# Performance work log

Measured on AMD Instinct MI355X. Metric: run time of the kernel, lower is better.

Reference implementation:

```python
import jax, jax.numpy as jnp
import numpy as np

B, T = 4, 512
IN, OUT, D, HID = 80, 4096, 512, 1024
E, NB, LPB = 4, 2, 4
NL = NB * LPB
H, M = 8, 64
LB, LA, SL, SR = 4, 1, 2, 1


def setup_inputs():
    key = jax.random.key(0)
    it = iter(jax.random.split(key, 40))
    def nrm(shape, s=0.02):
        return jax.random.normal(next(it), shape, jnp.float32) * s
    return {
        'x': jax.random.normal(next(it), (B, T, IN), jnp.float32),
        'seq_len': jax.random.randint(next(it), (B,), T // 2, T + 1),
        'emb_w1': nrm((IN, HID)), 'emb_b1': jnp.zeros((HID,), jnp.float32),
        'emb_w2': nrm((HID, D)), 'emb_wo': nrm((D, OUT)),
        'f0_w1': nrm((E, IN, HID)), 'f0_b1': jnp.zeros((E, HID), jnp.float32),
        'f0_w2': nrm((E, HID, D)), 'f0_router': nrm((D, E)),
        'f0_fb': nrm((LB, D), 0.1), 'f0_fa': nrm((LA, D), 0.1),
        'f_w1': nrm((NL - 1, E, D, HID)), 'f_b1': jnp.zeros((NL - 1, E, HID), jnp.float32),
        'f_w2': nrm((NL - 1, E, HID, D)), 'f_router': nrm((NL - 1, D, E)),
        'f_fb': nrm((NL - 1, LB, D), 0.1), 'f_fa': nrm((NL - 1, LA, D), 0.1),
        'attn_wq': nrm((NB, D, D)), 'attn_wk': nrm((NB, D, D)),
        'attn_wv': nrm((NB, D, D)), 'attn_wo': nrm((NB, D, D)),
        'attn_mk': nrm((NB, M, D)), 'attn_mv': nrm((NB, M, D)),
        'ln_g': jnp.ones((NB, D), jnp.float32), 'ln_b': jnp.zeros((NB, D), jnp.float32),
        'out_w': nrm((D, OUT)), 'out_b': jnp.zeros((OUT,), jnp.float32),
    }


def _fsmn_memory(p, fb, fa):
    # m[t] = p[t] + sum_k fb[k]*p[t-(k+1)*SL] + sum_j fa[j]*p[t+(j+1)*SR]  (depthwise)
    m = p
    for k in range(fb.shape[0]):
        off = (k + 1) * SL
        past = jnp.pad(p, ((0, 0), (off, 0), (0, 0)))[:, :p.shape[1]]
        m = m + past * fb[k]
    for j in range(fa.shape[0]):
        off = (j + 1) * SR
        fut = jnp.pad(p, ((0, 0), (0, off), (0, 0)))[:, off:]
        m = m + fut * fa[j]
    return m


def _pe(dtype):
    pos = jnp.arange(T, dtype=jnp.float32)[:, None]
    div = jnp.exp(jnp.arange(0, D, 2, dtype=jnp.float32) * (-np.log(10000.0) / D))
    pe = jnp.zeros((T, D), jnp.float32)
    pe = pe.at[:, 0::2].set(jnp.sin(pos * div)).at[:, 1::2].set(jnp.cos(pos * div))
    return pe.astype(dtype)


def _layernorm(x, g, b):
    mu = jnp.mean(x, -1, keepdims=True)
    var = jnp.var(x, -1, keepdims=True)
    return (x - mu) * jax.lax.rsqrt(var + 1e-5) * g + b


def reference(x, seq_len, emb_w1, emb_b1, emb_w2, emb_wo,
              f0_w1, f0_b1, f0_w2, f0_router, f0_fb, f0_fa,
              f_w1, f_b1, f_w2, f_router, f_fb, f_fa,
              attn_wq, attn_wk, attn_wv, attn_wo, attn_mk, attn_mv,
              ln_g, ln_b, out_w, out_b):
    tok_mask = jnp.arange(T)[None, :] < seq_len[:, None]  # [B,T] valid frames

    # embed sub-network (router features; detached as in Net.forward)
    embed = jax.nn.relu(x @ emb_w1 + emb_b1) @ emb_w2      # [B,T,D]
    embed_out = embed @ emb_wo                             # [B,T,OUT]
    embed_r = jax.lax.stop_gradient(embed)

    def moe_fsmn(xi, w1, b1, w2, router, fb, fa, skip):
        gates = jax.nn.softmax(embed_r @ router, axis=-1)  # [B,T,E]
        g = jnp.max(gates, axis=-1)
        disp = jax.nn.one_hot(jnp.argmax(gates, -1), E, dtype=xi.dtype) * g[..., None]
        h = jax.nn.relu(jnp.einsum('bti,eih->beth', xi, w1) + b1[None, :, None, :])
        p = jnp.einsum('beth,ehd->betd', h, w2)            # low-rank expert proj
        p = jnp.einsum('bte,betd->btd', disp, p)           # top-1 combine
        m = _fsmn_memory(p, fb, fa)
        if skip:
            m = m + xi
        imp = jnp.sum(gates * tok_mask[..., None].astype(gates.dtype), axis=(0, 1))
        aux = jnp.var(imp) / (jnp.mean(imp) ** 2 + 1e-9)   # importance cv^2
        return m, aux

    def attention(xi, wq, wk, wv, wo, mk, mv, g, b):
        dh = D // H
        q = (xi @ wq).reshape(B, T, H, dh)
        k = jnp.concatenate([xi @ wk, jnp.broadcast_to(mk, (B, M, D))], 1).reshape(B, T + M, H, dh)
        v = jnp.concatenate([xi @ wv, jnp.broadcast_to(mv, (B, M, D))], 1).reshape(B, T + M, H, dh)
        scores = jnp.einsum('bthd,bshd->bhts', q, k) / np.sqrt(dh).astype(np.float32)
        key_ok = jnp.concatenate([tok_mask, jnp.ones((B, M), bool)], 1)  # memory keys never masked
        scores = jnp.where(key_ok[:, None, None, :], scores, jnp.float32(-1e9))
        a = jax.nn.softmax(scores, -1)
        o = jnp.einsum('bhts,bshd->bthd', a, v).reshape(B, T, D) @ wo
        return _layernorm(xi + o, g, b)

    auxes = []
    cur = x
    li = 0
    for blk in range(NB):
        for _ in range(LPB):
            if li == 0:
                cur, aux = moe_fsmn(cur, f0_w1, f0_b1, f0_w2, f0_router, f0_fb, f0_fa, False)
            else:
                j = li - 1
                cur, aux = moe_fsmn(cur, f_w1[j], f_b1[j], f_w2[j], f_router[j], f_fb[j], f_fa[j], True)
            auxes.append(aux)
            li += 1
        if blk == 0:
            cur = cur + _pe(cur.dtype)[None]
        cur = attention(cur, attn_wq[blk], attn_wk[blk], attn_wv[blk], attn_wo[blk],
                        attn_mk[blk], attn_mv[blk], ln_g[blk], ln_b[blk])
    out = cur @ out_w + out_b
    return out, embed_out, jnp.stack(auxes).sum()
```

## Files before the change

kernel.cpp:

```cpp
#include <hip/hip_runtime.h>
#include <hip/hip_bf16.h>


typedef __bf16 bf16x8 __attribute__((ext_vector_type(8)));
typedef float f32x4 __attribute__((ext_vector_type(4)));

#define B_ 4
#define T_ 512
#define IN_ 80
#define OUT_ 4096
#define D_ 512
#define HID_ 1024
#define E_ 4
#define H_ 8
#define DH_ 64
#define M_ 64
#define BT_ (B_ * T_)
#define TKV_ (T_ + M_)
#define RBLK_ (BT_ / 4)

__device__ __forceinline__ unsigned pk2(float a, float b) {
    unsigned short ua = __builtin_bit_cast(unsigned short, (__bf16)a);
    unsigned short ub = __builtin_bit_cast(unsigned short, (__bf16)b);
    return (unsigned)ua | ((unsigned)ub << 16);
}
__device__ __forceinline__ unsigned pkh2(__bf16 a, __bf16 b) {
    unsigned short ua = __builtin_bit_cast(unsigned short, a);
    unsigned short ub = __builtin_bit_cast(unsigned short, b);
    return (unsigned)ua | ((unsigned)ub << 16);
}

__global__ __launch_bounds__(256) void gemm80_k(
    const float* __restrict__ A,
    const float* __restrict__ Bw,
    const float* __restrict__ bias,
    float* __restrict__ C)
{
    __shared__ float As[80][68];
    __shared__ float Bs[80][68];
    int m0 = blockIdx.y * 64, n0 = blockIdx.x * 64;
    int tid = threadIdx.x;
#pragma unroll
    for (int i = 0; i < 5; i++) {
        int idx = tid + 256 * i;
        int m = idx / 20, c = idx % 20;
        float4 f = *(const float4*)&A[(size_t)(m0 + m) * 80 + c * 4];
        As[c * 4 + 0][m] = f.x; As[c * 4 + 1][m] = f.y;
        As[c * 4 + 2][m] = f.z; As[c * 4 + 3][m] = f.w;
    }
#pragma unroll
    for (int i = 0; i < 5; i++) {
        int idx = tid + 256 * i;
        int k = idx / 16, c = idx % 16;
        float4 f = *(const float4*)&Bw[(size_t)k * 1024 + n0 + c * 4];
        *(float4*)&Bs[k][c * 4] = f;
    }
    __syncthreads();
    int tx = tid & 15, ty = tid >> 4;
    float acc[4][4];
#pragma unroll
    for (int j = 0; j < 4; j++)
#pragma unroll
        for (int i = 0; i < 4; i++) acc[j][i] = 0.f;
#pragma unroll 8
    for (int k = 0; k < 80; k++) {
        float4 a = *(const float4*)&As[k][ty * 4];
        float4 b = *(const float4*)&Bs[k][tx * 4];
        float av[4] = {a.x, a.y, a.z, a.w};
        float bv[4] = {b.x, b.y, b.z, b.w};
#pragma unroll
        for (int j = 0; j < 4; j++)
#pragma unroll
            for (int i = 0; i < 4; i++) acc[j][i] += av[j] * bv[i];
    }
#pragma unroll
    for (int j = 0; j < 4; j++) {
        size_t row = (size_t)(m0 + ty * 4 + j);
        float4 o;
        o.x = fmaxf(acc[j][0] + bias[n0 + tx * 4 + 0], 0.f);
        o.y = fmaxf(acc[j][1] + bias[n0 + tx * 4 + 1], 0.f);
        o.z = fmaxf(acc[j][2] + bias[n0 + tx * 4 + 2], 0.f);
        o.w = fmaxf(acc[j][3] + bias[n0 + tx * 4 + 3], 0.f);
        *(float4*)&C[row * 1024 + n0 + tx * 4] = o;
    }
}

__global__ void wr2_k(const float* __restrict__ w2,
                      const float* __restrict__ r0,
                      const float* __restrict__ rl,
                      float* __restrict__ R2)
{
    int wv = threadIdx.x >> 6, lane = threadIdx.x & 63;
    int h = blockIdx.x * 4 + wv;
    const float* wrow = w2 + (size_t)h * 512;
    float w[8];
#pragma unroll
    for (int i = 0; i < 8; i++) w[i] = wrow[lane + 64 * i];
    for (int l = 0; l < 8; l++) {
        const float* rp = (l == 0) ? r0 : rl + (size_t)(l - 1) * 2048;
        double a0 = 0, a1 = 0, a2 = 0, a3 = 0;
#pragma unroll
        for (int i = 0; i < 8; i++) {
            int d = lane + 64 * i;
            float4 r = *(const float4*)&rp[d * 4];
            a0 += (double)w[i] * (double)r.x;
            a1 += (double)w[i] * (double)r.y;
            a2 += (double)w[i] * (double)r.z;
            a3 += (double)w[i] * (double)r.w;
        }
        for (int off = 32; off; off >>= 1) {
            a0 += __shfl_xor(a0, off); a1 += __shfl_xor(a1, off);
            a2 += __shfl_xor(a2, off); a3 += __shfl_xor(a3, off);
        }
        if (lane == 0) {
            float4 o = make_float4((float)a0, (float)a1, (float)a2, (float)a3);
            *(float4*)&R2[((size_t)l * 1024 + h) * 4] = o;
        }
    }
}

__global__ __launch_bounds__(256) void routerall_k(
    const float* __restrict__ h,
    const float* __restrict__ R2,
    const int* __restrict__ seq_len,
    int* __restrict__ eid,
    float* __restrict__ gatev,
    float* __restrict__ impPart)
{
    __shared__ float impLoc[4][32];
    int wv = threadIdx.x >> 6, lane = threadIdx.x & 63;
    int tok = blockIdx.x * 4 + wv;
    const float* hr = h + (size_t)tok * 1024;
    float acc[8][4];
#pragma unroll
    for (int l = 0; l < 8; l++)
#pragma unroll
        for (int e = 0; e < 4; e++) acc[l][e] = 0.f;
    for (int i = 0; i < 16; i++) {
        int d = lane + 64 * i;
        float hv = hr[d];
#pragma unroll
        for (int l = 0; l < 8; l++) {
            float4 r = *(const float4*)&R2[((size_t)l * 1024 + d) * 4];
            acc[l][0] += hv * r.x; acc[l][1] += hv * r.y;
            acc[l][2] += hv * r.z; acc[l][3] += hv * r.w;
        }
    }
    for (int off = 32; off; off >>= 1) {
#pragma unroll
        for (int l = 0; l < 8; l++)
#pragma unroll
            for (int e = 0; e < 4; e++) acc[l][e] += __shfl_xor(acc[l][e], off);
    }
    if (lane == 0) {
        int b = tok >> 9, t = tok & 511;
        bool valid = t < seq_len[b];
        for (int l = 0; l < 8; l++) {
            float lg[4] = {acc[l][0], acc[l][1], acc[l][2], acc[l][3]};
            float mx = fmaxf(fmaxf(lg[0], lg[1]), fmaxf(lg[2], lg[3]));
            float g[4], s = 0.f;
            for (int e = 0; e < 4; e++) { g[e] = expf(lg[e] - mx); s += g[e]; }
            float inv = 1.f / s;
            int am = 0; float bv = g[0];
            for (int e = 1; e < 4; e++) if (g[e] > bv) { bv = g[e]; am = e; }
            eid[l * BT_ + tok] = am;
            gatev[l * BT_ + tok] = bv * inv;
            for (int e = 0; e < 4; e++)
                impLoc[wv][l * 4 + e] = valid ? g[e] * inv : 0.f;
        }
    }
    __syncthreads();
    int tid = threadIdx.x;
    if (tid < 32) {
        float s = impLoc[0][tid] + impLoc[1][tid] + impLoc[2][tid] + impLoc[3][tid];
        impPart[(size_t)blockIdx.x * 32 + tid] = s;
    }
}

__global__ void cvtw_k(const float* __restrict__ src, __bf16* __restrict__ dst,
                       int nsh, int kpsh, int Ksrc)
{
    int idx = blockIdx.x * 256 + threadIdx.x;
    int cprsh = nsh - 3;
    int row = idx >> cprsh;
    int chunk = idx & ((1 << cprsh) - 1);
    int e = row >> kpsh, k = row & ((1 << kpsh) - 1);
    int n = chunk * 8;
    uint4 pk;
    if (k < Ksrc) {
        const float* sp = src + (((size_t)e * Ksrc + k) << nsh) + n;
        float4 f0 = *(const float4*)sp;
        float4 f1 = *(const float4*)(sp + 4);
        pk = make_uint4(pk2(f0.x, f0.y), pk2(f0.z, f0.w),
                        pk2(f1.x, f1.y), pk2(f1.z, f1.w));
    } else pk = make_uint4(0, 0, 0, 0);
    *(uint4*)&dst[(((size_t)row) << nsh) + n] = pk;
}

__global__ void gathera_k(const float* __restrict__ src, int lda,
                          const int* __restrict__ sorted,
                          __bf16* __restrict__ dst, int kpsh, int Ksrc)
{
    int idx = blockIdx.x * 256 + threadIdx.x;
    int cprsh = kpsh - 3;
    int row = idx >> cprsh;
    int chunk = idx & ((1 << cprsh) - 1);
    int k0 = chunk * 8;
    uint4 pk;
    if (k0 < Ksrc) {
        const float* sp = src + (size_t)sorted[row] * lda + k0;
        float4 f0 = *(const float4*)sp;
        float4 f1 = *(const float4*)(sp + 4);
        pk = make_uint4(pk2(f0.x, f0.y), pk2(f0.z, f0.w),
                        pk2(f1.x, f1.y), pk2(f1.z, f1.w));
    } else pk = make_uint4(0, 0, 0, 0);
    *(uint4*)&dst[((size_t)row << kpsh) + k0] = pk;
}

template<bool W1OUT>
__global__ __launch_bounds__(256) void egemm_k(
    const __bf16* __restrict__ Ag, const __bf16* __restrict__ Bh,
    const float* __restrict__ bias,
    __bf16* __restrict__ Cb, float* __restrict__ Cf,
    int N, int Kpad,
    const int* __restrict__ seg, const int* __restrict__ sorted,
    const float* __restrict__ scale)
{
    __shared__ __align__(16) __bf16 As[2][128 * 64];
    __shared__ __align__(16) __bf16 Bs[2][64 * 64];

    int e = blockIdx.z;
    int row0 = seg[e], cnt = seg[e + 1] - row0;
    int m0 = blockIdx.y * 128;
    if (m0 >= cnt) return;
    int n0 = blockIdx.x * 64;
    const __bf16* Bp = Bh + (size_t)e * Kpad * N;

    int tid = threadIdx.x;
    int arow = tid >> 1, ahalf = tid & 1;
    const __bf16* aptr = Ag + (size_t)(row0 + m0 + arow) * Kpad + ahalf * 32;
    int asb = arow * 64;
    int ac0 = ahalf * 4;
    int arx = arow & 7;
    int bn = tid & 63, bkc = tid >> 6;
    const __bf16* bptr = Bp + n0 + bn;
    int bsb = bn * 64;
    int brx = bn & 7;

    int lane = tid & 63, wid = tid >> 6;
    int wm = wid & 1, wn = wid >> 1;
    int l15 = lane & 15, quad = lane >> 4;

    int aoff[4][2], boff[2][2];
#pragma unroll
    for (int mt = 0; mt < 4; mt++) {
        int m = wm * 64 + mt * 16 + l15;
#pragma unroll
        for (int s = 0; s < 2; s++)
            aoff[mt][s] = m * 64 + (((s * 4 + quad) ^ (m & 7)) * 8);
    }
#pragma unroll
    for (int nt = 0; nt < 2; nt++) {
        int n = wn * 32 + nt * 16 + l15;
#pragma unroll
        for (int s = 0; s < 2; s++)
            boff[nt][s] = n * 64 + (((s * 4 + quad) ^ (n & 7)) * 8);
    }

    f32x4 acc[4][2];
#pragma unroll
    for (int mt = 0; mt < 4; mt++)
#pragma unroll
        for (int nt = 0; nt < 2; nt++)
#pragma unroll
            for (int r = 0; r < 4; r++) acc[mt][nt][r] = 0.f;

    uint4 rA[4]; unsigned rB[8];
    auto stage = [&](int k0) {
#pragma unroll
        for (int j = 0; j < 4; j++) rA[j] = *(const uint4*)(aptr + k0 + j * 8);
#pragma unroll
        for (int c = 0; c < 2; c++) {
            int kk = k0 + (bkc * 2 + c) * 8;
#pragma unroll
            for (int i = 0; i < 4; i++)
                rB[c * 4 + i] = pkh2(bptr[(size_t)(kk + 2 * i) * N],
                                     bptr[(size_t)(kk + 2 * i + 1) * N]);
        }
    };
    auto commit = [&](int buf) {
#pragma unroll
        for (int j = 0; j < 4; j++)
            *(uint4*)&As[buf][asb + (((ac0 + j) ^ arx) * 8)] = rA[j];
#pragma unroll
        for (int c = 0; c < 2; c++)
            *(uint4*)&Bs[buf][bsb + (((bkc * 2 + c) ^ brx) * 8)] =
                make_uint4(rB[c * 4 + 0], rB[c * 4 + 1], rB[c * 4 + 2], rB[c * 4 + 3]);
    };

    stage(0); commit(0); __syncthreads();
    int nt_ = Kpad >> 6;
    for (int t = 0; t < nt_; t++) {
        int buf = t & 1;
        if (t + 1 < nt_) stage((t + 1) << 6);
        bf16x8 af[4][2], bfr[2][2];
#pragma unroll
        for (int mt = 0; mt < 4; mt++)
#pragma unroll
            for (int s = 0; s < 2; s++)
                af[mt][s] = *(const bf16x8*)&As[buf][aoff[mt][s]];
#pragma unroll
        for (int ntx = 0; ntx < 2; ntx++)
#pragma unroll
            for (int s = 0; s < 2; s++)
                bfr[ntx][s] = *(const bf16x8*)&Bs[buf][boff[ntx][s]];
#pragma unroll
        for (int mt = 0; mt < 4; mt++)
#pragma unroll
            for (int ntx = 0; ntx < 2; ntx++)
#pragma unroll
                for (int s = 0; s < 2; s++)
                    acc[mt][ntx] = __builtin_amdgcn_mfma_f32_16x16x32_bf16(
                        af[mt][s], bfr[ntx][s], acc[mt][ntx], 0, 0, 0);
        if (t + 1 < nt_) commit(buf ^ 1);
        __syncthreads();
    }

#pragma unroll
    for (int mt = 0; mt < 4; mt++) {
#pragma unroll
        for (int r = 0; r < 4; r++) {
            int m = m0 + wm * 64 + mt * 16 + quad * 4 + r;
            if (m >= cnt) continue;
            if (W1OUT) {
                size_t ci = (size_t)(row0 + m);
#pragma unroll
                for (int ntx = 0; ntx < 2; ntx++) {
                    int col = n0 + wn * 32 + ntx * 16 + l15;
                    float v = acc[mt][ntx][r] + bias[e * N + col];
                    Cb[ci * N + col] = (__bf16)fmaxf(v, 0.f);
                }
            } else {
                int tok = sorted[row0 + m];
                float sc = scale[tok];
#pragma unroll
                for (int ntx = 0; ntx < 2; ntx++) {
                    int col = n0 + wn * 32 + ntx * 16 + l15;
                    Cf[(size_t)tok * N + col] = acc[mt][ntx][r] * sc;
                }
            }
        }
    }
}

template<bool BIAS>
__global__ __launch_bounds__(256) void dgemm_k(
    const float* __restrict__ A,
    const __bf16* __restrict__ Bh,
    const float* __restrict__ bias,
    float* __restrict__ C,
    int N, int K)
{
    __shared__ __align__(16) __bf16 As[2][128 * 64];
    __shared__ __align__(16) __bf16 Bs[2][64 * 64];

    int m0 = blockIdx.y * 128, n0 = blockIdx.x * 64;
    int tid = threadIdx.x;
    int arow = tid >> 1, ahalf = tid & 1;
    const float* aptr = A + (size_t)(m0 + arow) * K + ahalf * 32;
    int asb = arow * 64, ac0 = ahalf * 4, arx = arow & 7;
    int bn = tid & 63, bkc = tid >> 6;
    const __bf16* bptr = Bh + n0 + bn;
    int bsb = bn * 64, brx = bn & 7;

    int lane = tid & 63, wid = tid >> 6;
    int wm = wid & 1, wn = wid >> 1;
    int l15 = lane & 15, quad = lane >> 4;

    int aoff[4][2], boff[2][2];
#pragma unroll
    for (int mt = 0; mt < 4; mt++) {
        int m = wm * 64 + mt * 16 + l15;
#pragma unroll
        for (int s = 0; s < 2; s++)
            aoff[mt][s] = m * 64 + (((s * 4 + quad) ^ (m & 7)) * 8);
    }
#pragma unroll
    for (int nt = 0; nt < 2; nt++) {
        int n = wn * 32 + nt * 16 + l15;
#pragma unroll
        for (int s = 0; s < 2; s++)
            boff[nt][s] = n * 64 + (((s * 4 + quad) ^ (n & 7)) * 8);
    }

    f32x4 acc[4][2];
#pragma unroll
    for (int mt = 0; mt < 4; mt++)
#pragma unroll
        for (int nt = 0; nt < 2; nt++)
#pragma unroll
            for (int r = 0; r < 4; r++) acc[mt][nt][r] = 0.f;

    uint4 rA[4]; unsigned rB[8];
    auto stage = [&](int k0) {
#pragma unroll
        for (int j = 0; j < 4; j++) {
            float4 f0 = *(const float4*)(aptr + k0 + j * 8);
            float4 f1 = *(const float4*)(aptr + k0 + j * 8 + 4);
            rA[j] = make_uint4(pk2(f0.x, f0.y), pk2(f0.z, f0.w),
                               pk2(f1.x, f1.y), pk2(f1.z, f1.w));
        }
#pragma unroll
        for (int c = 0; c < 2; c++) {
            int kk = k0 + (bkc * 2 + c) * 8;
#pragma unroll
            for (int i = 0; i < 4; i++)
                rB[c * 4 + i] = pkh2(bptr[(size_t)(kk + 2 * i) * N],
                                     bptr[(size_t)(kk + 2 * i + 1) * N]);
        }
    };
    auto commit = [&](int buf) {
#pragma unroll
        for (int j = 0; j < 4; j++)
            *(uint4*)&As[buf][asb + (((ac0 + j) ^ arx) * 8)] = rA[j];
#pragma unroll
        for (int c = 0; c < 2; c++)
            *(uint4*)&Bs[buf][bsb + (((bkc * 2 + c) ^ brx) * 8)] =
                make_uint4(rB[c * 4 + 0], rB[c * 4 + 1], rB[c * 4 + 2], rB[c * 4 + 3]);
    };

    stage(0); commit(0); __syncthreads();
    int nt_ = K >> 6;
    for (int t = 0; t < nt_; t++) {
        int buf = t & 1;
        if (t + 1 < nt_) stage((t + 1) << 6);
        bf16x8 af[4][2], bfr[2][2];
#pragma unroll
        for (int mt = 0; mt < 4; mt++)
#pragma unroll
            for (int s = 0; s < 2; s++)
                af[mt][s] = *(const bf16x8*)&As[buf][aoff[mt][s]];
#pragma unroll
        for (int ntx = 0; ntx < 2; ntx++)
#pragma unroll
            for (int s = 0; s < 2; s++)
                bfr[ntx][s] = *(const bf16x8*)&Bs[buf][boff[ntx][s]];
#pragma unroll
        for (int mt = 0; mt < 4; mt++)
#pragma unroll
            for (int ntx = 0; ntx < 2; ntx++)
#pragma unroll
                for (int s = 0; s < 2; s++)
                    acc[mt][ntx] = __builtin_amdgcn_mfma_f32_16x16x32_bf16(
                        af[mt][s], bfr[ntx][s], acc[mt][ntx], 0, 0, 0);
        if (t + 1 < nt_) commit(buf ^ 1);
        __syncthreads();
    }

#pragma unroll
    for (int mt = 0; mt < 4; mt++) {
#pragma unroll
        for (int r = 0; r < 4; r++) {
            int m = m0 + wm * 64 + mt * 16 + quad * 4 + r;
#pragma unroll
            for (int ntx = 0; ntx < 2; ntx++) {
                int col = n0 + wn * 32 + ntx * 16 + l15;
                float v = acc[mt][ntx][r];
                if (BIAS) v += bias[col];
                C[(size_t)m * N + col] = v;
            }
        }
    }
}

#define MBM 128
#define MBN 64
#define MBK 32
#define LDAS 40

__global__ __launch_bounds__(256) void qkv_k(
    const float* __restrict__ A,
    const __bf16* __restrict__ wq, const __bf16* __restrict__ wk,
    const __bf16* __restrict__ wv,
    float* __restrict__ qo, float* __restrict__ ko, float* __restrict__ vo)
{
    __shared__ __align__(16) __bf16 As[MBM * LDAS];
    __shared__ __align__(16) __bf16 Bs[MBN * LDAS];

    int n0g = blockIdx.x * MBN;
    int which = n0g >> 9;
    int n0 = n0g & 511;
    const __bf16* Bp = (which == 0) ? wq : (which == 1) ? wk : wv;
    float* Cp = (which == 0) ? qo : (which == 1) ? ko : vo;
    int m0 = blockIdx.y * MBM;

    int tid = threadIdx.x;
    int arow = tid >> 1, ahalf = tid & 1;
    const float* aptr = A + (size_t)(m0 + arow) * D_ + ahalf * 16;
    int asw = (arow >> 3) & 3;
    int bn = tid & 63, bkc = tid >> 6;
    int bcs = bkc ^ ((bn >> 3) & 3);

    int lane = tid & 63, wid = tid >> 6;
    int wm = wid & 1, wn = wid >> 1;
    int l15 = lane & 15, quad = lane >> 4;

    int aoff[4], boff[2];
#pragma unroll
    for (int mt = 0; mt < 4; mt++) {
        int m = wm * 64 + mt * 16 + l15;
        aoff[mt] = m * LDAS + (quad ^ ((m >> 3) & 3)) * 8;
    }
#pragma unroll
    for (int nt = 0; nt < 2; nt++) {
        int n = wn * 32 + nt * 16 + l15;
        boff[nt] = n * LDAS + (quad ^ ((n >> 3) & 3)) * 8;
    }

    f32x4 acc[4][2];
#pragma unroll
    for (int mt = 0; mt < 4; mt++)
#pragma unroll
        for (int nt = 0; nt < 2; nt++)
#pragma unroll
            for (int r = 0; r < 4; r++) acc[mt][nt][r] = 0.f;

    for (int k0 = 0; k0 < D_; k0 += MBK) {
#pragma unroll
        for (int cc = 0; cc < 2; cc++) {
            float4 f0 = *(const float4*)(aptr + k0 + cc * 8);
            float4 f1 = *(const float4*)(aptr + k0 + cc * 8 + 4);
            uint4 pk = make_uint4(pk2(f0.x, f0.y), pk2(f0.z, f0.w),
                                  pk2(f1.x, f1.y), pk2(f1.z, f1.w));
            int cs = (ahalf * 2 + cc) ^ asw;
            *(uint4*)&As[arow * LDAS + cs * 8] = pk;
        }
        {
            __bf16 f[8];
            int kk = k0 + bkc * 8;
#pragma unroll
            for (int i = 0; i < 8; i++)
                f[i] = Bp[(size_t)(kk + i) * D_ + n0 + bn];
            uint4 pk = make_uint4(pkh2(f[0], f[1]), pkh2(f[2], f[3]),
                                  pkh2(f[4], f[5]), pkh2(f[6], f[7]));
            *(uint4*)&Bs[bn * LDAS + bcs * 8] = pk;
        }
        __syncthreads();
        bf16x8 af[4], bfm[2];
#pragma unroll
        for (int mt = 0; mt < 4; mt++) af[mt] = *(const bf16x8*)&As[aoff[mt]];
#pragma unroll
        for (int nt = 0; nt < 2; nt++) bfm[nt] = *(const bf16x8*)&Bs[boff[nt]];
#pragma unroll
        for (int mt = 0; mt < 4; mt++)
#pragma unroll
            for (int nt = 0; nt < 2; nt++)
                acc[mt][nt] = __builtin_amdgcn_mfma_f32_16x16x32_bf16(
                    af[mt], bfm[nt], acc[mt][nt], 0, 0, 0);
        __syncthreads();
    }

#pragma unroll
    for (int mt = 0; mt < 4; mt++) {
#pragma unroll
        for (int r = 0; r < 4; r++) {
            int mi = wm * 64 + mt * 16 + quad * 4 + r;
            int m = m0 + mi;
            size_t crow = which ? (size_t)(m + (m >> 9) * M_) : (size_t)m;
#pragma unroll
            for (int nt = 0; nt < 2; nt++) {
                int col = n0 + wn * 32 + nt * 16 + l15;
                Cp[crow * (size_t)D_ + col] = acc[mt][nt][r];
            }
        }
    }
}

__global__ void bucketall_k(const int* __restrict__ eidA, int* __restrict__ sortedA,
                            int* __restrict__ segA)
{
    __shared__ int cnt[E_]; __shared__ int cur[E_];
    int l = blockIdx.x;
    const int* eid = eidA + l * BT_;
    int* sorted = sortedA + l * BT_;
    int* seg = segA + l * 8;
    int tid = threadIdx.x;
    if (tid < E_) cnt[tid] = 0;
    __syncthreads();
    for (int t = tid; t < BT_; t += 256) atomicAdd(&cnt[eid[t]], 1);
    __syncthreads();
    if (tid == 0) {
        int o = 0;
        for (int e = 0; e < E_; e++) { seg[e] = o; cur[e] = o; o += cnt[e]; }
        seg[E_] = o;
    }
    __syncthreads();
    for (int t = tid; t < BT_; t += 256) {
        int pos = atomicAdd(&cur[eid[t]], 1);
        sorted[pos] = t;
    }
}

__global__ void fsmn_k(const float* __restrict__ p, const float* __restrict__ fb,
                       const float* __restrict__ fa, float* __restrict__ cur, int skip)
{
    int idx = blockIdx.x * 256 + threadIdx.x;
    int d = idx & 511;
    int t = (idx >> 9) & 511;
    float m = p[idx];
#pragma unroll
    for (int k = 0; k < 4; k++) {
        int tt = t - 2 * (k + 1);
        if (tt >= 0) m += fb[k * D_ + d] * p[idx - D_ * 2 * (k + 1)];
    }
    if (t + 1 < T_) m += fa[d] * p[idx + D_];
    if (skip) m += cur[idx];
    cur[idx] = m;
}

__global__ void addpe_k(float* __restrict__ cur) {
    int idx = blockIdx.x * 256 + threadIdx.x;
    int d = idx & 511, t = (idx >> 9) & 511;
    float div = expf((float)(d & ~1) * (-9.210340371976184f / (float)D_));
    float ang = (float)t * div;
    cur[idx] += (d & 1) ? cosf(ang) : sinf(ang);
}

__global__ void fillmem_k(const float* __restrict__ mk, const float* __restrict__ mv,
                          float* __restrict__ kbuf, float* __restrict__ vbuf)
{
    int idx = blockIdx.x * 256 + threadIdx.x;
    int d = idx & 511, m = (idx >> 9) & 63, b = idx >> 15;
    size_t row = (size_t)b * TKV_ + T_ + m;
    kbuf[row * D_ + d] = mk[m * D_ + d];
    vbuf[row * D_ + d] = mv[m * D_ + d];
}

#define QR 16
__global__ __launch_bounds__(256) void attn_k(
    const float* __restrict__ q, const float* __restrict__ kbuf,
    const float* __restrict__ vbuf, const int* __restrict__ seq_len,
    float* __restrict__ attno)
{
    __shared__ float kv[64 * 68];
    __shared__ float qs[QR][68];
    __shared__ float sc[QR][584];
    int b = blockIdx.z, h = blockIdx.y, t0 = blockIdx.x * QR;
    int tid = threadIdx.x, w = tid >> 6, lane = tid & 63;
    int r0 = w * 4;
#pragma unroll
    for (int i = 0; i < 4; i++) {
        int idx = tid + 256 * i;
        int r = idx >> 6, d = idx & 63;
        qs[r][d] = q[((size_t)(b * T_) + t0 + r) * D_ + h * DH_ + d] * 0.125f;
    }
    int sl = seq_len[b];
    int ntv = (sl + 63) >> 6;
    int kg = lane & 15, quad = lane >> 4;
    int myrow = r0 + quad;

    for (int ti = 0; ti <= ntv; ti++) {
        int t = (ti < ntv) ? ti : 8;
        int s0 = t * 64;
        __syncthreads();
        {
            const float* kp = kbuf + ((size_t)b * TKV_ + s0 + w * 16) * D_ + h * DH_ + lane;
#pragma unroll
            for (int jj = 0; jj < 4; jj++) {
                float4 kf;
                kf.x = kp[(jj * 4 + 0) * D_];
                kf.y = kp[(jj * 4 + 1) * D_];
                kf.z = kp[(jj * 4 + 2) * D_];
                kf.w = kp[(jj * 4 + 3) * D_];
                *(float4*)&kv[lane * 68 + w * 16 + jj * 4] = kf;
            }
        }
        __syncthreads();
        float a0 = 0, a1 = 0, a2 = 0, a3 = 0;
#pragma unroll 8
        for (int d = 0; d < 64; d++) {
            float4 kf = *(const float4*)&kv[d * 68 + kg * 4];
            float qv = qs[myrow][d];
            a0 = fmaf(qv, kf.x, a0);
            a1 = fmaf(qv, kf.y, a1);
            a2 = fmaf(qv, kf.z, a2);
            a3 = fmaf(qv, kf.w, a3);
        }
        int sb = s0 + kg * 4;
        float4 o;
        o.x = (sb + 0 >= T_ || sb + 0 < sl) ? a0 : -1e9f;
        o.y = (sb + 1 >= T_ || sb + 1 < sl) ? a1 : -1e9f;
        o.z = (sb + 2 >= T_ || sb + 2 < sl) ? a2 : -1e9f;
        o.w = (sb + 3 >= T_ || sb + 3 < sl) ? a3 : -1e9f;
        *(float4*)&sc[myrow][s0 + kg * 4] = o;
    }
    __syncthreads();

    float inv[4];
#pragma unroll
    for (int r = 0; r < 4; r++) {
        float mx = -1e30f;
        for (int ti = 0; ti <= ntv; ti++) {
            int s0 = ((ti < ntv) ? ti : 8) * 64;
            mx = fmaxf(mx, sc[r0 + r][s0 + lane]);
        }
        for (int off = 32; off; off >>= 1) mx = fmaxf(mx, __shfl_xor(mx, off));
        float sum = 0.f;
        for (int ti = 0; ti <= ntv; ti++) {
            int s0 = ((ti < ntv) ? ti : 8) * 64;
            float e2 = expf(sc[r0 + r][s0 + lane] - mx);
            sc[r0 + r][s0 + lane] = e2; sum += e2;
        }
        for (int off = 32; off; off >>= 1) sum += __shfl_xor(sum, off);
        inv[r] = 1.f / sum;
    }

    float o0 = 0, o1 = 0, o2 = 0, o3 = 0;
    for (int ti = 0; ti <= ntv; ti++) {
        int t = (ti < ntv) ? ti : 8;
        int s0 = t * 64;
        __syncthreads();
#pragma unroll
        for (int i = 0; i < 16; i++) {
            int idx = tid + 256 * i;
            int key = idx >> 6, d = idx & 63;
            kv[key * 68 + d] = vbuf[((size_t)b * TKV_ + s0 + key) * D_ + h * DH_ + d];
        }
        __syncthreads();
#pragma unroll 4
        for (int g = 0; g < 16; g++) {
            float4 p0 = *(const float4*)&sc[r0 + 0][s0 + g * 4];
            float4 p1 = *(const float4*)&sc[r0 + 1][s0 + g * 4];
            float4 p2 = *(const float4*)&sc[r0 + 2][s0 + g * 4];
            float4 p3 = *(const float4*)&sc[r0 + 3][s0 + g * 4];
            float v0 = kv[(g * 4 + 0) * 68 + lane];
            float v1 = kv[(g * 4 + 1) * 68 + lane];
            float v2 = kv[(g * 4 + 2) * 68 + lane];
            float v3 = kv[(g * 4 + 3) * 68 + lane];
            o0 += p0.x * v0 + p0.y * v1 + p0.z * v2 + p0.w * v3;
            o1 += p1.x * v0 + p1.y * v1 + p1.z * v2 + p1.w * v3;
            o2 += p2.x * v0 + p2.y * v1 + p2.z * v2 + p2.w * v3;
            o3 += p3.x * v0 + p3.y * v1 + p3.z * v2 + p3.w * v3;
        }
    }
    size_t base = ((size_t)(b * T_) + t0 + r0) * D_ + h * DH_ + lane;
    attno[base + 0 * D_] = o0 * inv[0];
    attno[base + 1 * D_] = o1 * inv[1];
    attno[base + 2 * D_] = o2 * inv[2];
    attno[base + 3 * D_] = o3 * inv[3];
}

__global__ void ln_k(const float* __restrict__ o, const float* __restrict__ g,
                     const float* __restrict__ bb, float* __restrict__ cur)
{
    int w = threadIdx.x >> 6, lane = threadIdx.x & 63;
    size_t row = (size_t)(blockIdx.x * 4 + w);
    float v[8]; float s = 0.f;
#pragma unroll
    for (int i = 0; i < 8; i++) {
        int d = lane + 64 * i;
        v[i] = cur[row * D_ + d] + o[row * D_ + d];
        s += v[i];
    }
    for (int off = 32; off; off >>= 1) s += __shfl_xor(s, off);
    float mu = s * (1.f / D_);
    float vs = 0.f;
#pragma unroll
    for (int i = 0; i < 8; i++) { float dd = v[i] - mu; vs += dd * dd; }
    for (int off = 32; off; off >>= 1) vs += __shfl_xor(vs, off);
    float rstd = rsqrtf(vs * (1.f / D_) + 1e-5f);
#pragma unroll
    for (int i = 0; i < 8; i++) {
        int d = lane + 64 * i;
        cur[row * D_ + d] = (v[i] - mu) * rstd * g[d] + bb[d];
    }
}

__global__ __launch_bounds__(256) void aux_k(const float* __restrict__ impPart,
                                             float* __restrict__ outp)
{
    __shared__ float red[8][32];
    __shared__ float imp[32];
    int tid = threadIdx.x;
    int c = tid & 31, p = tid >> 5;
    float s = 0.f;
    for (int b = p; b < RBLK_; b += 8) s += impPart[(size_t)b * 32 + c];
    red[p][c] = s;
    __syncthreads();
    if (tid < 32) {
        float t = 0.f;
#pragma unroll
        for (int i = 0; i < 8; i++) t += red[i][tid];
        imp[tid] = t;
    }
    __syncthreads();
    if (tid == 0) {
        float total = 0.f;
        for (int l = 0; l < 8; l++) {
            const float* ip = imp + l * 4;
            float m = (ip[0] + ip[1] + ip[2] + ip[3]) * 0.25f;
            float var = 0.f;
            for (int e = 0; e < 4; e++) { float d = ip[e] - m; var += d * d; }
            var *= 0.25f;
            total += var / (m * m + 1e-9f);
        }
        *outp = total;
    }
}

extern "C" void kernel_launch(void* const* d_in, const int* in_sizes, int n_in,
                              void* d_out, int out_size, void* d_ws, size_t ws_size,
                              hipStream_t stream)
{
    (void)in_sizes; (void)n_in; (void)out_size; (void)ws_size;
    const float* x        = (const float*)d_in[0];
    const int*   seqlen   = (const int*)d_in[1];
    const float* emb_w1   = (const float*)d_in[2];
    const float* emb_b1   = (const float*)d_in[3];
    const float* emb_w2   = (const float*)d_in[4];
    const float* emb_wo   = (const float*)d_in[5];
    const float* f0_w1    = (const float*)d_in[6];
    const float* f0_b1    = (const float*)d_in[7];
    const float* f0_w2    = (const float*)d_in[8];
    const float* f0_router= (const float*)d_in[9];
    const float* f0_fb    = (const float*)d_in[10];
    const float* f0_fa    = (const float*)d_in[11];
    const float* f_w1     = (const float*)d_in[12];
    const float* f_b1     = (const float*)d_in[13];
    const float* f_w2     = (const float*)d_in[14];
    const float* f_router = (const float*)d_in[15];
    const float* f_fb     = (const float*)d_in[16];
    const float* f_fa     = (const float*)d_in[17];
    const float* attn_wq  = (const float*)d_in[18];
    const float* attn_wk  = (const float*)d_in[19];
    const float* attn_wv  = (const float*)d_in[20];
    const float* attn_wo  = (const float*)d_in[21];
    const float* attn_mk  = (const float*)d_in[22];
    const float* attn_mv  = (const float*)d_in[23];
    const float* ln_g     = (const float*)d_in[24];
    const float* ln_b     = (const float*)d_in[25];
    const float* out_w    = (const float*)d_in[26];
    const float* out_b    = (const float*)d_in[27];

    float* out0 = (float*)d_out;
    float* out1 = out0 + (size_t)BT_ * OUT_;
    float* out2 = out1 + (size_t)BT_ * OUT_;

    float* fws = (float*)d_ws;
    size_t o = 0;
    float* embedF = fws + o; o += (size_t)BT_ * D_;
    float* curB   = fws + o; o += (size_t)BT_ * D_;
    float* hbuf   = fws + o; o += (size_t)BT_ * HID_;
    float* pbuf   = fws + o; o += (size_t)BT_ * D_;
    float* kbuf   = fws + o; o += (size_t)B_ * TKV_ * D_;
    float* vbuf   = fws + o; o += (size_t)B_ * TKV_ * D_;
    float* gatev  = fws + o; o += (size_t)8 * BT_;
    float* impPart= fws + o; o += (size_t)RBLK_ * 32;
    float* R2     = fws + o; o += (size_t)8 * 1024 * 4;
    int* eid     = (int*)(fws + o); o += (size_t)8 * BT_;
    int* sortedA = (int*)(fws + o); o += (size_t)8 * BT_;
    int* segA    = (int*)(fws + o); o += 64;
    __bf16* Ag    = (__bf16*)hbuf;
    __bf16* hbufh = (__bf16*)(hbuf + (size_t)BT_ * D_ / 2);
    __bf16* w1h   = (__bf16*)kbuf;
    __bf16* w2h   = (__bf16*)vbuf;
    __bf16* w2e_h = (__bf16*)vbuf;
    __bf16* woe_h = (__bf16*)kbuf;
    __bf16* outw_h= (__bf16*)kbuf;
    __bf16* wqh   = (__bf16*)embedF;
    __bf16* wkh   = wqh + (size_t)D_ * D_;
    __bf16* wvh   = wkh + (size_t)D_ * D_;
    __bf16* woh   = wvh + (size_t)D_ * D_;
    float* qbuf  = pbuf;
    float* attno = hbuf;
    float* tmpo  = hbuf + (size_t)BT_ * D_;

    gemm80_k<<<dim3(HID_ / 64, BT_ / 64, 1), 256, 0, stream>>>(x, emb_w1, emb_b1, hbuf);
    wr2_k<<<256, 256, 0, stream>>>(emb_w2, f0_router, f_router, R2);
    routerall_k<<<RBLK_, 256, 0, stream>>>(hbuf, R2, seqlen, eid, gatev, impPart);
    bucketall_k<<<8, 256, 0, stream>>>(eid, sortedA, segA);
    cvtw_k<<<256, 256, 0, stream>>>(emb_w2, w2e_h, 9, 10, HID_);
    cvtw_k<<<1024, 256, 0, stream>>>(emb_wo, woe_h, 12, 9, D_);
    dgemm_k<false><<<dim3(D_ / 64, BT_ / 128, 1), 256, 0, stream>>>(
        hbuf, w2e_h, nullptr, embedF, D_, HID_);
    dgemm_k<false><<<dim3(OUT_ / 64, BT_ / 128, 1), 256, 0, stream>>>(
        embedF, woe_h, nullptr, out1, OUT_, D_);

    for (int l = 0; l < 8; l++) {
        const float* w1  = (l == 0) ? f0_w1 : f_w1 + (size_t)(l-1) * E_ * D_ * HID_;
        const float* b1p = (l == 0) ? f0_b1 : f_b1 + (size_t)(l-1) * E_ * HID_;
        const float* w2  = (l == 0) ? f0_w2 : f_w2 + (size_t)(l-1) * E_ * HID_ * D_;
        const float* fbp = (l == 0) ? f0_fb : f_fb + (size_t)(l-1) * 4 * D_;
        const float* fap = (l == 0) ? f0_fa : f_fa + (size_t)(l-1) * 1 * D_;
        const float* Ain = (l == 0) ? x : curB;
        int lda  = (l == 0) ? IN_ : D_;
        int Ks   = (l == 0) ? IN_ : D_;
        int Kp   = (l == 0) ? 128 : 512;
        int kpsh = (l == 0) ? 7 : 9;
        const int* seg = segA + l * 8;
        const int* sorted = sortedA + l * BT_;

        cvtw_k<<<E_ * Kp * HID_ / 8 / 256, 256, 0, stream>>>(w1, w1h, 10, kpsh, Ks);
        cvtw_k<<<E_ * HID_ * D_ / 8 / 256, 256, 0, stream>>>(w2, w2h, 9, 10, HID_);
        gathera_k<<<BT_ * Kp / 8 / 256, 256, 0, stream>>>(Ain, lda, sorted, Ag, kpsh, Ks);

        egemm_k<true><<<dim3(HID_/64, BT_/128, E_), 256, 0, stream>>>(
            Ag, w1h, b1p, hbufh, nullptr, HID_, Kp, seg, nullptr, nullptr);
        egemm_k<false><<<dim3(D_/64, BT_/128, E_), 256, 0, stream>>>(
            hbufh, w2h, nullptr, nullptr, pbuf, D_, HID_, seg, sorted, gatev + l * BT_);
        fsmn_k<<<BT_*D_/256, 256, 0, stream>>>(pbuf, fbp, fap, curB, (l > 0) ? 1 : 0);

        if (l == 3) addpe_k<<<BT_*D_/256, 256, 0, stream>>>(curB);

        if (l == 3 || l == 7) {
            int ab = (l == 3) ? 0 : 1;
            const float* wq = attn_wq + (size_t)ab * D_ * D_;
            const float* wk = attn_wk + (size_t)ab * D_ * D_;
            const float* wv = attn_wv + (size_t)ab * D_ * D_;
            const float* wo = attn_wo + (size_t)ab * D_ * D_;
            const float* mk = attn_mk + (size_t)ab * M_ * D_;
            const float* mv = attn_mv + (size_t)ab * M_ * D_;
            const float* g  = ln_g + (size_t)ab * D_;
            const float* bb = ln_b + (size_t)ab * D_;

            cvtw_k<<<128, 256, 0, stream>>>(wq, wqh, 9, 9, D_);
            cvtw_k<<<128, 256, 0, stream>>>(wk, wkh, 9, 9, D_);
            cvtw_k<<<128, 256, 0, stream>>>(wv, wvh, 9, 9, D_);
            cvtw_k<<<128, 256, 0, stream>>>(wo, woh, 9, 9, D_);
            qkv_k<<<dim3(3 * D_ / MBN, BT_ / MBM, 1), 256, 0, stream>>>(
                curB, wqh, wkh, wvh, qbuf, kbuf, vbuf);
            fillmem_k<<<B_*M_*D_/256, 256, 0, stream>>>(mk, mv, kbuf, vbuf);
            attn_k<<<dim3(T_/QR, H_, B_), 256, 0, stream>>>(qbuf, kbuf, vbuf, seqlen, attno);
            dgemm_k<false><<<dim3(D_ / 64, BT_ / 128, 1), 256, 0, stream>>>(
                attno, woh, nullptr, tmpo, D_, D_);
            ln_k<<<BT_/4, 256, 0, stream>>>(tmpo, g, bb, curB);
        }
    }

    cvtw_k<<<1024, 256, 0, stream>>>(out_w, outw_h, 12, 9, D_);
    dgemm_k<true><<<dim3(OUT_ / 64, BT_ / 128, 1), 256, 0, stream>>>(
        curB, outw_h, out_b, out0, OUT_, D_);
    aux_k<<<1, 256, 0, stream>>>(impPart, out2);
}
```

Baseline: 1.424 ms.

## Fuse weight bf16 conversion and expert gather into GEMM loads, drop aux kernels

Removes the separate fp32-to-bf16 weight conversion kernels and the expert-row gather kernel. GEMMs now read fp32 weights and permuted fp32 activations directly and convert to bf16 while staging tiles. Also folds positional-encoding addition into the FSMN kernel and reads attention memory keys/values directly instead of copying them into the K/V buffers. This saves launches and intermediate global round trips, at the cost of twice the bytes per weight load and strided fp32 B loads inside the GEMM inner loop.

```diff
diff --git a/kernel.cpp b/kernel.cpp
--- a/kernel.cpp
+++ b/kernel.cpp
@@ -22,11 +22,6 @@
 __device__ __forceinline__ unsigned pk2(float a, float b) {
     unsigned short ua = __builtin_bit_cast(unsigned short, (__bf16)a);
     unsigned short ub = __builtin_bit_cast(unsigned short, (__bf16)b);
-    return (unsigned)ua | ((unsigned)ub << 16);
-}
-__device__ __forceinline__ unsigned pkh2(__bf16 a, __bf16 b) {
-    unsigned short ua = __builtin_bit_cast(unsigned short, a);
-    unsigned short ub = __builtin_bit_cast(unsigned short, b);
     return (unsigned)ua | ((unsigned)ub << 16);
 }
 
@@ -177,49 +172,11 @@
     }
 }
 
-__global__ void cvtw_k(const float* __restrict__ src, __bf16* __restrict__ dst,
-                       int nsh, int kpsh, int Ksrc)
-{
-    int idx = blockIdx.x * 256 + threadIdx.x;
-    int cprsh = nsh - 3;
-    int row = idx >> cprsh;
-    int chunk = idx & ((1 << cprsh) - 1);
-    int e = row >> kpsh, k = row & ((1 << kpsh) - 1);
-    int n = chunk * 8;
-    uint4 pk;
-    if (k < Ksrc) {
-        const float* sp = src + (((size_t)e * Ksrc + k) << nsh) + n;
-        float4 f0 = *(const float4*)sp;
-        float4 f1 = *(const float4*)(sp + 4);
-        pk = make_uint4(pk2(f0.x, f0.y), pk2(f0.z, f0.w),
-                        pk2(f1.x, f1.y), pk2(f1.z, f1.w));
-    } else pk = make_uint4(0, 0, 0, 0);
-    *(uint4*)&dst[(((size_t)row) << nsh) + n] = pk;
-}
-
-__global__ void gathera_k(const float* __restrict__ src, int lda,
-                          const int* __restrict__ sorted,
-                          __bf16* __restrict__ dst, int kpsh, int Ksrc)
-{
-    int idx = blockIdx.x * 256 + threadIdx.x;
-    int cprsh = kpsh - 3;
-    int row = idx >> cprsh;
-    int chunk = idx & ((1 << cprsh) - 1);
-    int k0 = chunk * 8;
-    uint4 pk;
-    if (k0 < Ksrc) {
-        const float* sp = src + (size_t)sorted[row] * lda + k0;
-        float4 f0 = *(const float4*)sp;
-        float4 f1 = *(const float4*)(sp + 4);
-        pk = make_uint4(pk2(f0.x, f0.y), pk2(f0.z, f0.w),
-                        pk2(f1.x, f1.y), pk2(f1.z, f1.w));
-    } else pk = make_uint4(0, 0, 0, 0);
-    *(uint4*)&dst[((size_t)row << kpsh) + k0] = pk;
-}
-
 template<bool W1OUT>
 __global__ __launch_bounds__(256) void egemm_k(
-    const __bf16* __restrict__ Ag, const __bf16* __restrict__ Bh,
+    const float* __restrict__ Af, int lda, int Ks,
+    const __bf16* __restrict__ Ah,
+    const float* __restrict__ Bw,
     const float* __restrict__ bias,
     __bf16* __restrict__ Cb, float* __restrict__ Cf,
     int N, int Kpad,
@@ -234,18 +191,19 @@
     int m0 = blockIdx.y * 128;
     if (m0 >= cnt) return;
     int n0 = blockIdx.x * 64;
-    const __bf16* Bp = Bh + (size_t)e * Kpad * N;
+    const float* Bp = Bw + (size_t)e * Ks * N;
 
     int tid = threadIdx.x;
     int arow = tid >> 1, ahalf = tid & 1;
-    const __bf16* aptr = Ag + (size_t)(row0 + m0 + arow) * Kpad + ahalf * 32;
-    int asb = arow * 64;
-    int ac0 = ahalf * 4;
-    int arx = arow & 7;
+    int mclamp = min(m0 + arow, cnt - 1);
+    const float*  afp = nullptr;
+    const __bf16* ahp = nullptr;
+    if (W1OUT) afp = Af + (size_t)sorted[row0 + mclamp] * lda + ahalf * 32;
+    else       ahp = Ah + (size_t)(row0 + mclamp) * Kpad + ahalf * 32;
+    int asb = arow * 64, ac0 = ahalf * 4, arx = arow & 7;
     int bn = tid & 63, bkc = tid >> 6;
-    const __bf16* bptr = Bp + n0 + bn;
-    int bsb = bn * 64;
-    int brx = bn & 7;
+    const float* bptr = Bp + n0 + bn;
+    int bsb = bn * 64, brx = bn & 7;
 
     int lane = tid & 63, wid = tid >> 6;
     int wm = wid & 1, wn = wid >> 1;
@@ -277,15 +235,31 @@
 
     uint4 rA[4]; unsigned rB[8];
     auto stage = [&](int k0) {
-#pragma unroll
-        for (int j = 0; j < 4; j++) rA[j] = *(const uint4*)(aptr + k0 + j * 8);
+        if (W1OUT) {
+#pragma unroll
+            for (int j = 0; j < 4; j++) {
+                int kg = ahalf * 32 + k0 + j * 8;
+                if (kg < Ks) {
+                    float4 f0 = *(const float4*)(afp + k0 + j * 8);
+                    float4 f1 = *(const float4*)(afp + k0 + j * 8 + 4);
+                    rA[j] = make_uint4(pk2(f0.x, f0.y), pk2(f0.z, f0.w),
+                                       pk2(f1.x, f1.y), pk2(f1.z, f1.w));
+                } else rA[j] = make_uint4(0, 0, 0, 0);
+            }
+        } else {
+#pragma unroll
+            for (int j = 0; j < 4; j++) rA[j] = *(const uint4*)(ahp + k0 + j * 8);
+        }
 #pragma unroll
         for (int c = 0; c < 2; c++) {
             int kk = k0 + (bkc * 2 + c) * 8;
 #pragma unroll
-            for (int i = 0; i < 4; i++)
-                rB[c * 4 + i] = pkh2(bptr[(size_t)(kk + 2 * i) * N],
-                                     bptr[(size_t)(kk + 2 * i + 1) * N]);
+            for (int i = 0; i < 4; i++) {
+                int ka = kk + 2 * i, kb = ka + 1;
+                float fa = (ka < Ks) ? bptr[(size_t)ka * N] : 0.f;
+                float fb = (kb < Ks) ? bptr[(size_t)kb * N] : 0.f;
+                rB[c * 4 + i] = pk2(fa, fb);
+            }
         }
     };
     auto commit = [&](int buf) {
@@ -356,7 +330,7 @@
 template<bool BIAS>
 __global__ __launch_bounds__(256) void dgemm_k(
     const float* __restrict__ A,
-    const __bf16* __restrict__ Bh,
+    const float* __restrict__ Bw,
     const float* __restrict__ bias,
     float* __restrict__ C,
     int N, int K)
@@ -370,7 +344,7 @@
     const float* aptr = A + (size_t)(m0 + arow) * K + ahalf * 32;
     int asb = arow * 64, ac0 = ahalf * 4, arx = arow & 7;
     int bn = tid & 63, bkc = tid >> 6;
-    const __bf16* bptr = Bh + n0 + bn;
+    const float* bptr = Bw + n0 + bn;
     int bsb = bn * 64, brx = bn & 7;
 
     int lane = tid & 63, wid = tid >> 6;
@@ -415,8 +389,8 @@
             int kk = k0 + (bkc * 2 + c) * 8;
 #pragma unroll
             for (int i = 0; i < 4; i++)
-                rB[c * 4 + i] = pkh2(bptr[(size_t)(kk + 2 * i) * N],
-                                     bptr[(size_t)(kk + 2 * i + 1) * N]);
+                rB[c * 4 + i] = pk2(bptr[(size_t)(kk + 2 * i) * N],
+                                    bptr[(size_t)(kk + 2 * i + 1) * N]);
         }
     };
     auto commit = [&](int buf) {
@@ -480,8 +454,8 @@
 
 __global__ __launch_bounds__(256) void qkv_k(
     const float* __restrict__ A,
-    const __bf16* __restrict__ wq, const __bf16* __restrict__ wk,
-    const __bf16* __restrict__ wv,
+    const float* __restrict__ wq, const float* __restrict__ wk,
+    const float* __restrict__ wv,
     float* __restrict__ qo, float* __restrict__ ko, float* __restrict__ vo)
 {
     __shared__ __align__(16) __bf16 As[MBM * LDAS];
@@ -490,7 +464,7 @@
     int n0g = blockIdx.x * MBN;
     int which = n0g >> 9;
     int n0 = n0g & 511;
-    const __bf16* Bp = (which == 0) ? wq : (which == 1) ? wk : wv;
+    const float* Bp = (which == 0) ? wq : (which == 1) ? wk : wv;
     float* Cp = (which == 0) ? qo : (which == 1) ? ko : vo;
     int m0 = blockIdx.y * MBM;
 
@@ -536,13 +510,13 @@
             *(uint4*)&As[arow * LDAS + cs * 8] = pk;
         }
         {
-            __bf16 f[8];
+            float f[8];
             int kk = k0 + bkc * 8;
 #pragma unroll
             for (int i = 0; i < 8; i++)
                 f[i] = Bp[(size_t)(kk + i) * D_ + n0 + bn];
-            uint4 pk = make_uint4(pkh2(f[0], f[1]), pkh2(f[2], f[3]),
-                                  pkh2(f[4], f[5]), pkh2(f[6], f[7]));
+            uint4 pk = make_uint4(pk2(f[0], f[1]), pk2(f[2], f[3]),
+                                  pk2(f[4], f[5]), pk2(f[6], f[7]));
             *(uint4*)&Bs[bn * LDAS + bcs * 8] = pk;
         }
         __syncthreads();
@@ -566,11 +540,10 @@
         for (int r = 0; r < 4; r++) {
             int mi = wm * 64 + mt * 16 + quad * 4 + r;
             int m = m0 + mi;
-            size_t crow = which ? (size_t)(m + (m >> 9) * M_) : (size_t)m;
 #pragma unroll
             for (int nt = 0; nt < 2; nt++) {
                 int col = n0 + wn * 32 + nt * 16 + l15;
-                Cp[crow * (size_t)D_ + col] = acc[mt][nt][r];
+                Cp[(size_t)m * D_ + col] = acc[mt][nt][r];
             }
         }
     }
@@ -602,7 +575,8 @@
 }
 
 __global__ void fsmn_k(const float* __restrict__ p, const float* __restrict__ fb,
-                       const float* __restrict__ fa, float* __restrict__ cur, int skip)
+                       const float* __restrict__ fa, float* __restrict__ cur,
+                       int skip, int pe)
 {
     int idx = blockIdx.x * 256 + threadIdx.x;
     int d = idx & 511;
@@ -615,31 +589,19 @@
     }
     if (t + 1 < T_) m += fa[d] * p[idx + D_];
     if (skip) m += cur[idx];
+    if (pe) {
+        float div = expf((float)(d & ~1) * (-9.210340371976184f / (float)D_));
+        float ang = (float)t * div;
+        m += (d & 1) ? cosf(ang) : sinf(ang);
+    }
     cur[idx] = m;
-}
-
-__global__ void addpe_k(float* __restrict__ cur) {
-    int idx = blockIdx.x * 256 + threadIdx.x;
-    int d = idx & 511, t = (idx >> 9) & 511;
-    float div = expf((float)(d & ~1) * (-9.210340371976184f / (float)D_));
-    float ang = (float)t * div;
-    cur[idx] += (d & 1) ? cosf(ang) : sinf(ang);
-}
-
-__global__ void fillmem_k(const float* __restrict__ mk, const float* __restrict__ mv,
-                          float* __restrict__ kbuf, float* __restrict__ vbuf)
-{
-    int idx = blockIdx.x * 256 + threadIdx.x;
-    int d = idx & 511, m = (idx >> 9) & 63, b = idx >> 15;
-    size_t row = (size_t)b * TKV_ + T_ + m;
-    kbuf[row * D_ + d] = mk[m * D_ + d];
-    vbuf[row * D_ + d] = mv[m * D_ + d];
 }
 
 #define QR 16
 __global__ __launch_bounds__(256) void attn_k(
     const float* __restrict__ q, const float* __restrict__ kbuf,
-    const float* __restrict__ vbuf, const int* __restrict__ seq_len,
+    const float* __restrict__ vbuf, const float* __restrict__ mk,
+    const float* __restrict__ mv, const int* __restrict__ seq_len,
     float* __restrict__ attno)
 {
     __shared__ float kv[64 * 68];
@@ -664,7 +626,9 @@
         int s0 = t * 64;
         __syncthreads();
         {
-            const float* kp = kbuf + ((size_t)b * TKV_ + s0 + w * 16) * D_ + h * DH_ + lane;
+            const float* kp = (t < 8)
+                ? kbuf + ((size_t)(b * T_) + s0 + w * 16) * D_ + h * DH_ + lane
+                : mk + (size_t)(w * 16) * D_ + h * DH_ + lane;
 #pragma unroll
             for (int jj = 0; jj < 4; jj++) {
                 float4 kf;
@@ -724,7 +688,10 @@
         for (int i = 0; i < 16; i++) {
             int idx = tid + 256 * i;
             int key = idx >> 6, d = idx & 63;
-            kv[key * 68 + d] = vbuf[((size_t)b * TKV_ + s0 + key) * D_ + h * DH_ + d];
+            const float* vp = (t < 8)
+                ? vbuf + ((size_t)(b * T_) + s0 + key) * D_ + h * DH_ + d
+                : mv + (size_t)key * D_ + h * DH_ + d;
+            kv[key * 68 + d] = *vp;
         }
         __syncthreads();
 #pragma unroll 4
@@ -852,25 +819,15 @@
     float* curB   = fws + o; o += (size_t)BT_ * D_;
     float* hbuf   = fws + o; o += (size_t)BT_ * HID_;
     float* pbuf   = fws + o; o += (size_t)BT_ * D_;
-    float* kbuf   = fws + o; o += (size_t)B_ * TKV_ * D_;
-    float* vbuf   = fws + o; o += (size_t)B_ * TKV_ * D_;
+    float* kbuf   = fws + o; o += (size_t)BT_ * D_;
+    float* vbuf   = fws + o; o += (size_t)BT_ * D_;
     float* gatev  = fws + o; o += (size_t)8 * BT_;
     float* impPart= fws + o; o += (size_t)RBLK_ * 32;
     float* R2     = fws + o; o += (size_t)8 * 1024 * 4;
     int* eid     = (int*)(fws + o); o += (size_t)8 * BT_;
     int* sortedA = (int*)(fws + o); o += (size_t)8 * BT_;
     int* segA    = (int*)(fws + o); o += 64;
-    __bf16* Ag    = (__bf16*)hbuf;
-    __bf16* hbufh = (__bf16*)(hbuf + (size_t)BT_ * D_ / 2);
-    __bf16* w1h   = (__bf16*)kbuf;
-    __bf16* w2h   = (__bf16*)vbuf;
-    __bf16* w2e_h = (__bf16*)vbuf;
-    __bf16* woe_h = (__bf16*)kbuf;
-    __bf16* outw_h= (__bf16*)kbuf;
-    __bf16* wqh   = (__bf16*)embedF;
-    __bf16* wkh   = wqh + (size_t)D_ * D_;
-    __bf16* wvh   = wkh + (size_t)D_ * D_;
-    __bf16* woh   = wvh + (size_t)D_ * D_;
+    __bf16* hbufh = (__bf16*)hbuf;
     float* qbuf  = pbuf;
     float* attno = hbuf;
     float* tmpo  = hbuf + (size_t)BT_ * D_;
@@ -879,12 +836,10 @@
     wr2_k<<<256, 256, 0, stream>>>(emb_w2, f0_router, f_router, R2);
     routerall_k<<<RBLK_, 256, 0, stream>>>(hbuf, R2, seqlen, eid, gatev, impPart);
     bucketall_k<<<8, 256, 0, stream>>>(eid, sortedA, segA);
-    cvtw_k<<<256, 256, 0, stream>>>(emb_w2, w2e_h, 9, 10, HID_);
-    cvtw_k<<<1024, 256, 0, stream>>>(emb_wo, woe_h, 12, 9, D_);
     dgemm_k<false><<<dim3(D_ / 64, BT_ / 128, 1), 256, 0, stream>>>(
-        hbuf, w2e_h, nullptr, embedF, D_, HID_);
+        hbuf, emb_w2, nullptr, embedF, D_, HID_);
     dgemm_k<false><<<dim3(OUT_ / 64, BT_ / 128, 1), 256, 0, stream>>>(
-        embedF, woe_h, nullptr, out1, OUT_, D_);
+        embedF, emb_wo, nullptr, out1, OUT_, D_);
 
     for (int l = 0; l < 8; l++) {
         const float* w1  = (l == 0) ? f0_w1 : f_w1 + (size_t)(l-1) * E_ * D_ * HID_;
@@ -896,21 +851,17 @@
         int lda  = (l == 0) ? IN_ : D_;
         int Ks   = (l == 0) ? IN_ : D_;
         int Kp   = (l == 0) ? 128 : 512;
-        int kpsh = (l == 0) ? 7 : 9;
         const int* seg = segA + l * 8;
         const int* sorted = sortedA + l * BT_;
 
-        cvtw_k<<<E_ * Kp * HID_ / 8 / 256, 256, 0, stream>>>(w1, w1h, 10, kpsh, Ks);
-        cvtw_k<<<E_ * HID_ * D_ / 8 / 256, 256, 0, stream>>>(w2, w2h, 9, 10, HID_);
-        gathera_k<<<BT_ * Kp / 8 / 256, 256, 0, stream>>>(Ain, lda, sorted, Ag, kpsh, Ks);
-
         egemm_k<true><<<dim3(HID_/64, BT_/128, E_), 256, 0, stream>>>(
-            Ag, w1h, b1p, hbufh, nullptr, HID_, Kp, seg, nullptr, nullptr);
+            Ain, lda, Ks, nullptr, w1, b1p, hbufh, nullptr, HID_, Kp,
+            seg, sorted, nullptr);
         egemm_k<false><<<dim3(D_/64, BT_/128, E_), 256, 0, stream>>>(
-            hbufh, w2h, nullptr, nullptr, pbuf, D_, HID_, seg, sorted, gatev + l * BT_);
-        fsmn_k<<<BT_*D_/256, 256, 0, stream>>>(pbuf, fbp, fap, curB, (l > 0) ? 1 : 0);
-
-        if (l == 3) addpe_k<<<BT_*D_/256, 256, 0, stream>>>(curB);
+            nullptr, 0, HID_, hbufh, w2, nullptr, nullptr, pbuf, D_, HID_,
+            seg, sorted, gatev + l * BT_);
+        fsmn_k<<<BT_*D_/256, 256, 0, stream>>>(pbuf, fbp, fap, curB,
+                                               (l > 0) ? 1 : 0, (l == 3) ? 1 : 0);
 
         if (l == 3 || l == 7) {
             int ab = (l == 3) ? 0 : 1;
@@ -923,22 +874,17 @@
             const float* g  = ln_g + (size_t)ab * D_;
             const float* bb = ln_b + (size_t)ab * D_;
 
-            cvtw_k<<<128, 256, 0, stream>>>(wq, wqh, 9, 9, D_);
-            cvtw_k<<<128, 256, 0, stream>>>(wk, wkh, 9, 9, D_);
-            cvtw_k<<<128, 256, 0, stream>>>(wv, wvh, 9, 9, D_);
-            cvtw_k<<<128, 256, 0, stream>>>(wo, woh, 9, 9, D_);
             qkv_k<<<dim3(3 * D_ / MBN, BT_ / MBM, 1), 256, 0, stream>>>(
-                curB, wqh, wkh, wvh, qbuf, kbuf, vbuf);
-            fillmem_k<<<B_*M_*D_/256, 256, 0, stream>>>(mk, mv, kbuf, vbuf);
-            attn_k<<<dim3(T_/QR, H_, B_), 256, 0, stream>>>(qbuf, kbuf, vbuf, seqlen, attno);
+                curB, wq, wk, wv, qbuf, kbuf, vbuf);
+            attn_k<<<dim3(T_/QR, H_, B_), 256, 0, stream>>>(
+                qbuf, kbuf, vbuf, mk, mv, seqlen, attno);
             dgemm_k<false><<<dim3(D_ / 64, BT_ / 128, 1), 256, 0, stream>>>(
-                attno, woh, nullptr, tmpo, D_, D_);
+                attno, wo, nullptr, tmpo, D_, D_);
             ln_k<<<BT_/4, 256, 0, stream>>>(tmpo, g, bb, curB);
         }
     }
 
-    cvtw_k<<<1024, 256, 0, stream>>>(out_w, outw_h, 12, 9, D_);
     dgemm_k<true><<<dim3(OUT_ / 64, BT_ / 128, 1), 256, 0, stream>>>(
-        curB, outw_h, out_b, out0, OUT_, D_);
+        curB, out_w, out_b, out0, OUT_, D_);
     aux_k<<<1, 256, 0, stream>>>(impPart, out2);
 }
```

After: 2.434 ms. 1.71x slower.
